# Kernel optimization log

Hardware: AMD Instinct MI355X
Metric: run time of the kernel (lower is better)

Reference implementation:

```python
import jax, jax.numpy as jnp
import numpy as np

N_NODES = 50000
N_EDGES = 400000
D = 64          # in_feats == out_feats (transform=False)
DIST_DIM = 32
NUM = 5         # num_neighbor
N_BOUND = 64    # embedding table rows = N_BOUND + 1


def setup_inputs() -> dict:
    key = jax.random.key(0)
    ks = jax.random.split(key, 9)
    feat = jax.random.normal(ks[0], (N_NODES, D), dtype=jnp.float32)
    loc = jax.random.uniform(ks[1], (N_NODES, 2), dtype=jnp.float32)
    embed_table = jax.random.normal(ks[2], (N_BOUND + 1, DIST_DIM), dtype=jnp.float32)
    G_w = jax.random.normal(ks[3], (D, DIST_DIM), dtype=jnp.float32) / np.sqrt(DIST_DIM)
    agg_w = jax.random.normal(ks[4], (D, 2 * D), dtype=jnp.float32) / np.sqrt(2 * D)
    agg_b = jnp.zeros((D,), dtype=jnp.float32)
    boundaries = jnp.linspace(0.0, 2.0, N_BOUND).astype(jnp.float32)
    src = jax.random.randint(ks[5], (N_EDGES,), 0, N_NODES, dtype=jnp.int32)
    dst = jax.random.randint(ks[6], (N_EDGES,), 0, N_NODES, dtype=jnp.int32)
    inter_ids = jax.random.randint(ks[7], (N_EDGES, NUM), 0, N_NODES, dtype=jnp.int32)
    return {"feat": feat, "loc": loc, "embed_table": embed_table, "G_w": G_w,
            "agg_w": agg_w, "agg_b": agg_b, "boundaries": boundaries,
            "src": src, "dst": dst, "inter_ids": inter_ids}


def reference(feat, loc, embed_table, G_w, agg_w, agg_b, boundaries, src, dst, inter_ids):
    n = feat.shape[0]
    e, num = inter_ids.shape
    one = jnp.ones((e,), dtype=jnp.float32)
    # degrees: d0 = in_deg^-0.5 (at dst), d2 = out_deg^-0.5 (at src), clamp(min=1)
    in_deg = jnp.maximum(jax.ops.segment_sum(one, dst, num_segments=n), 1.0)
    out_deg = jnp.maximum(jax.ops.segment_sum(one, src, num_segments=n), 1.0)
    d0 = in_deg ** -0.5  # [N]
    d2 = out_deg ** -0.5  # [N]
    # dist1: dst->src node distance per edge
    loc_src = loc[src]                                   # [E,2]
    dist1 = jnp.linalg.norm(loc[dst] - loc_src, axis=1)  # [E]
    # dist_: src to each sampled intermediate node
    inter_pos = loc[inter_ids]                                     # [E,num,2]
    dist_ = jnp.linalg.norm(loc_src[:, None, :] - inter_pos, axis=-1)  # [E,num]
    # bucketize (torch right=False == searchsorted side='left') -> embed -> linear G
    b1 = jnp.searchsorted(boundaries, dist1, side='left')   # [E]
    b_ = jnp.searchsorted(boundaries, dist_, side='left')   # [E,num]
    dist_embed1 = embed_table[b1] @ G_w.T                    # [E,D]
    dist_embed_ = embed_table[b_] @ G_w.T                    # [E,num,D]
    # mean over sampled intermediates of (dist-embed * gathered feat)
    dist_embed_dot_h = (dist_embed_ * feat[inter_ids]).mean(axis=1)  # [E,D]
    # agg_fc on concat, degree-scaled
    cat = jnp.concatenate([dist_embed1 * feat[src], dist_embed_dot_h], axis=1)  # [E,2D]
    h = (d0[dst] * d2[src])[:, None] * (cat @ agg_w.T + agg_b)                  # [E,D]
    # copy_e / sum: scatter-sum edges to dst nodes
    rst = jax.ops.segment_sum(h, dst, num_segments=n)  # [N,D]
    return rst
```

## Files before the change

kernel.cpp:

```cpp
#include <hip/hip_runtime.h>


#define DFEAT 64

typedef __attribute__((ext_vector_type(8))) short short8;
typedef __attribute__((ext_vector_type(4))) float floatx4;

__device__ __forceinline__ short bf16h(float x) {
    unsigned u = __float_as_uint(x);
    return (short)((u + 0x7FFFu + ((u >> 16) & 1u)) >> 16);
}
__device__ __forceinline__ float bf16tof(short h) {
    return __uint_as_float(((unsigned)(unsigned short)h) << 16);
}

__device__ __forceinline__ void sb8(const signed char* p, float (&f)[8]) {
    int2 q = *(const int2*)p;
#pragma unroll
    for (int t = 0; t < 4; ++t) f[t] = (float)((q.x << (24 - 8 * t)) >> 24);
#pragma unroll
    for (int t = 0; t < 4; ++t) f[4 + t] = (float)((q.y << (24 - 8 * t)) >> 24);
}

__device__ __forceinline__ int bucketize(float x, float bnd) {
    int i = (int)(x * 31.5f);
    i = min(max(i, 0), 64);
#pragma unroll
    for (int t = 0; t < 3; ++t) {
        float bi = __shfl(bnd, min(i, 63));
        if (i < 64 && bi < x) ++i;
    }
#pragma unroll
    for (int t = 0; t < 2; ++t) {
        float bim = __shfl(bnd, max(i - 1, 0));
        if (i > 0 && bim >= x) --i;
    }
    return i;
}

__global__ void k_init(const float* __restrict__ Etab,
                       const float* __restrict__ G, float* __restrict__ P,
                       float* __restrict__ rst, float* __restrict__ degs,
                       int nRst, int nDeg) {
    int i = blockIdx.x * blockDim.x + threadIdx.x;
    if (i < nRst) rst[i] = 0.0f;
    if (i < nDeg) degs[i] = 0.0f;
    if (i < 65 * DFEAT) {
        int b = i >> 6, o = i & 63;
        float a = 0.0f;
#pragma unroll
        for (int m = 0; m < 32; ++m)
            a = fmaf(Etab[b * 32 + m], G[o * 32 + m], a);
        P[i] = a;
    }
}

__global__ void k_quant(const float* __restrict__ feat,
                        signed char* __restrict__ featQ,
                        float* __restrict__ scaleQ, int N) {
    int w = (blockIdx.x * blockDim.x + threadIdx.x) >> 6;
    int lane = threadIdx.x & 63;
    if (w >= N) return;
    float f = feat[(w << 6) + lane];
    float a = fabsf(f);
#pragma unroll
    for (int o = 32; o; o >>= 1) a = fmaxf(a, __shfl_xor(a, o));
    float inv = (a > 0.0f) ? 127.0f / a : 0.0f;
    int q = __float2int_rn(f * inv);
    featQ[(w << 6) + lane] = (signed char)q;
    if (lane == 0) scaleQ[w] = a * (1.0f / 127.0f);
}

__global__ void k_deg(const int* __restrict__ src, const int* __restrict__ dst,
                      float* __restrict__ degs, int N, int E) {
    int i = blockIdx.x * blockDim.x + threadIdx.x;
    if (i < E) {
        atomicAdd(&degs[dst[i]], 1.0f);
        atomicAdd(&degs[N + src[i]], 1.0f);
    }
}

#define PPAD 68

__global__ __launch_bounds__(256, 3) void k_edge(
    const float* __restrict__ feat, const signed char* __restrict__ featQ,
    const float* __restrict__ scaleQ, const float* __restrict__ loc,
    const float* __restrict__ agg_w, const float* __restrict__ agg_b,
    const float* __restrict__ bnds, const int* __restrict__ src,
    const int* __restrict__ dst, const int* __restrict__ inter,
    const float* __restrict__ P, const float* __restrict__ degs,
    float* __restrict__ rst, int N, int E) {
    const int tid = threadIdx.x;
    const int lane = tid & 63;
    const int wid = tid >> 6;
    const int m16 = lane & 15;
    const int quad = lane >> 4;

    __shared__ float sP[65 * PPAD];
    __shared__ short8 sWBh[16 * 64];
    __shared__ short8 sWBl[16 * 64];

    for (int i = tid; i < 65 * DFEAT; i += 256)
        sP[(i >> 6) * PPAD + (i & 63)] = P[i];

    for (int f = wid; f < 16; f += 4) {
        int sl = f >> 2, nt = f & 3;
        const float* wp = agg_w + (nt * 16 + m16) * 128 + sl * 32 + quad * 8;
        floatx4 wa = *(const floatx4*)wp;
        floatx4 wb = *(const floatx4*)(wp + 4);
        float xs[8] = {wa.x, wa.y, wa.z, wa.w, wb.x, wb.y, wb.z, wb.w};
        short8 h, l;
#pragma unroll
        for (int j = 0; j < 8; ++j) {
            short hh = bf16h(xs[j]);
            h[j] = hh;
            l[j] = bf16h(xs[j] - bf16tof(hh));
        }
        sWBh[f * 64 + lane] = h;
        sWBl[f * 64 + lane] = l;
    }

    const float bnd = bnds[lane];
    float bias4[4];
#pragma unroll
    for (int nt = 0; nt < 4; ++nt) bias4[nt] = agg_b[nt * 16 + m16];

    __syncthreads();

    const int nstream = gridDim.x << 2;
    const int wstream = (blockIdx.x << 2) + wid;
    const int ngroups = (E + 15) >> 4;

    for (int g = wstream; g < ngroups; g += nstream) {
        const int em = (g << 4) + m16;
        const bool act = em < E;
        const int ec = act ? em : 0;

        const int s = __builtin_nontemporal_load(src + ec);
        const int d = __builtin_nontemporal_load(dst + ec);
        const float2 ls = ((const float2*)loc)[s];
        const float2 ld = ((const float2*)loc)[d];
        float dsc = rsqrtf(fmaxf(degs[d], 1.0f)) *
                    rsqrtf(fmaxf(degs[N + s], 1.0f));
        if (!act) dsc = 0.0f;

        float dx = ld.x - ls.x, dy = ld.y - ls.y;
        const int b1 = bucketize(sqrtf(dx * dx + dy * dy), bnd);

        int ij[5], bj[5];
        float sq[5];
#pragma unroll
        for (int j = 0; j < 5; ++j) {
            int id = __builtin_nontemporal_load(inter + ec * 5 + j);
            ij[j] = id;
            if (featQ) sq[j] = scaleQ[id];
            float2 lj = ((const float2*)loc)[id];
            float ex = ls.x - lj.x, ey = ls.y - lj.y;
            bj[j] = bucketize(sqrtf(ex * ex + ey * ey), bnd);
        }

        short8 Ah[4], Al[4];
        if (featQ) {
            const float ssrc = scaleQ[s];
            const signed char* qrow = featQ + (s << 6);
            const float* prow = sP + b1 * PPAD;
#pragma unroll
            for (int sl = 0; sl < 2; ++sl) {
                int k0 = sl * 32 + quad * 8;
                float fq[8];
                sb8(qrow + k0, fq);
                floatx4 pa = *(const floatx4*)(prow + k0);
                floatx4 pb = *(const floatx4*)(prow + k0 + 4);
                float xs[8] = {fq[0] * ssrc * pa.x, fq[1] * ssrc * pa.y,
                               fq[2] * ssrc * pa.z, fq[3] * ssrc * pa.w,
                               fq[4] * ssrc * pb.x, fq[5] * ssrc * pb.y,
                               fq[6] * ssrc * pb.z, fq[7] * ssrc * pb.w};
                short8 h, l;
#pragma unroll
                for (int j = 0; j < 8; ++j) {
                    short hh = bf16h(xs[j]);
                    h[j] = hh;
                    l[j] = bf16h(xs[j] - bf16tof(hh));
                }
                Ah[sl] = h;
                Al[sl] = l;
            }
#pragma unroll
            for (int sl = 0; sl < 2; ++sl) {
                int k0 = sl * 32 + quad * 8;
                float r[8] = {0, 0, 0, 0, 0, 0, 0, 0};
#pragma unroll
                for (int j = 0; j < 5; ++j) {
                    float fq[8];
                    sb8(featQ + (ij[j] << 6) + k0, fq);
                    const float sj = sq[j];
                    const float* pr = sP + bj[j] * PPAD;
                    floatx4 pa = *(const floatx4*)(pr + k0);
                    floatx4 pb = *(const floatx4*)(pr + k0 + 4);
                    r[0] = fmaf(fq[0] * sj, pa.x, r[0]);
                    r[1] = fmaf(fq[1] * sj, pa.y, r[1]);
                    r[2] = fmaf(fq[2] * sj, pa.z, r[2]);
                    r[3] = fmaf(fq[3] * sj, pa.w, r[3]);
                    r[4] = fmaf(fq[4] * sj, pb.x, r[4]);
                    r[5] = fmaf(fq[5] * sj, pb.y, r[5]);
                    r[6] = fmaf(fq[6] * sj, pb.z, r[6]);
                    r[7] = fmaf(fq[7] * sj, pb.w, r[7]);
                }
                short8 h, l;
#pragma unroll
                for (int j = 0; j < 8; ++j) {
                    float x = r[j] * 0.2f;
                    short hh = bf16h(x);
                    h[j] = hh;
                    l[j] = bf16h(x - bf16tof(hh));
                }
                Ah[2 + sl] = h;
                Al[2 + sl] = l;
            }
        } else {
            const float* frow = feat + (s << 6);
            const float* prow = sP + b1 * PPAD;
#pragma unroll
            for (int sl = 0; sl < 2; ++sl) {
                int k0 = sl * 32 + quad * 8;
                floatx4 fa = *(const floatx4*)(frow + k0);
                floatx4 fb = *(const floatx4*)(frow + k0 + 4);
                floatx4 pa = *(const floatx4*)(prow + k0);
                floatx4 pb = *(const floatx4*)(prow + k0 + 4);
                float xs[8] = {fa.x * pa.x, fa.y * pa.y, fa.z * pa.z,
                               fa.w * pa.w, fb.x * pb.x, fb.y * pb.y,
                               fb.z * pb.z, fb.w * pb.w};
                short8 h, l;
#pragma unroll
                for (int j = 0; j < 8; ++j) {
                    short hh = bf16h(xs[j]);
                    h[j] = hh;
                    l[j] = bf16h(xs[j] - bf16tof(hh));
                }
                Ah[sl] = h;
                Al[sl] = l;
            }
#pragma unroll
            for (int sl = 0; sl < 2; ++sl) {
                int k0 = sl * 32 + quad * 8;
                float r[8] = {0, 0, 0, 0, 0, 0, 0, 0};
#pragma unroll
                for (int j = 0; j < 5; ++j) {
                    const float* fr = feat + (ij[j] << 6);
                    const float* pr = sP + bj[j] * PPAD;
                    floatx4 fa = *(const floatx4*)(fr + k0);
                    floatx4 fb = *(const floatx4*)(fr + k0 + 4);
                    floatx4 pa = *(const floatx4*)(pr + k0);
                    floatx4 pb = *(const floatx4*)(pr + k0 + 4);
                    r[0] = fmaf(fa.x, pa.x, r[0]);
                    r[1] = fmaf(fa.y, pa.y, r[1]);
                    r[2] = fmaf(fa.z, pa.z, r[2]);
                    r[3] = fmaf(fa.w, pa.w, r[3]);
                    r[4] = fmaf(fb.x, pb.x, r[4]);
                    r[5] = fmaf(fb.y, pb.y, r[5]);
                    r[6] = fmaf(fb.z, pb.z, r[6]);
                    r[7] = fmaf(fb.w, pb.w, r[7]);
                }
                short8 h, l;
#pragma unroll
                for (int j = 0; j < 8; ++j) {
                    float x = r[j] * 0.2f;
                    short hh = bf16h(x);
                    h[j] = hh;
                    l[j] = bf16h(x - bf16tof(hh));
                }
                Ah[2 + sl] = h;
                Al[2 + sl] = l;
            }
        }

        floatx4 acc[4] = {{0, 0, 0, 0}, {0, 0, 0, 0}, {0, 0, 0, 0}, {0, 0, 0, 0}};
#pragma unroll
        for (int sl = 0; sl < 4; ++sl) {
#pragma unroll
            for (int nt = 0; nt < 4; ++nt) {
                short8 bh = sWBh[((sl << 2) + nt) * 64 + lane];
                short8 bl = sWBl[((sl << 2) + nt) * 64 + lane];
                acc[nt] = __builtin_amdgcn_mfma_f32_16x16x32_bf16(
                    Ah[sl], bh, acc[nt], 0, 0, 0);
                acc[nt] = __builtin_amdgcn_mfma_f32_16x16x32_bf16(
                    Al[sl], bh, acc[nt], 0, 0, 0);
                acc[nt] = __builtin_amdgcn_mfma_f32_16x16x32_bf16(
                    Ah[sl], bl, acc[nt], 0, 0, 0);
            }
        }

#pragma unroll
        for (int r = 0; r < 4; ++r) {
            const int m = (quad << 2) + r;
            const int dm = __shfl(d, m);
            const float sc = __shfl(dsc, m);
            float* ap = rst + (dm << 6) + m16;
            float v0 = (acc[0][r] + bias4[0]) * sc;
            float v1 = (acc[1][r] + bias4[1]) * sc;
            float v2 = (acc[2][r] + bias4[2]) * sc;
            float v3 = (acc[3][r] + bias4[3]) * sc;
            asm volatile("global_atomic_add_f32 %0, %1, off nt"
                         :: "v"(ap), "v"(v0) : "memory");
            asm volatile("global_atomic_add_f32 %0, %1, off offset:64 nt"
                         :: "v"(ap), "v"(v1) : "memory");
            asm volatile("global_atomic_add_f32 %0, %1, off offset:128 nt"
                         :: "v"(ap), "v"(v2) : "memory");
            asm volatile("global_atomic_add_f32 %0, %1, off offset:192 nt"
                         :: "v"(ap), "v"(v3) : "memory");
        }
    }
}

extern "C" void kernel_launch(void* const* d_in, const int* in_sizes, int n_in,
                              void* d_out, int out_size, void* d_ws,
                              size_t ws_size, hipStream_t stream) {
    const float* feat  = (const float*)d_in[0];
    const float* loc   = (const float*)d_in[1];
    const float* embed = (const float*)d_in[2];
    const float* G_w   = (const float*)d_in[3];
    const float* agg_w = (const float*)d_in[4];
    const float* agg_b = (const float*)d_in[5];
    const float* bnds  = (const float*)d_in[6];
    const int* src   = (const int*)d_in[7];
    const int* dst   = (const int*)d_in[8];
    const int* inter = (const int*)d_in[9];

    const int N = in_sizes[0] / DFEAT;
    const int E = in_sizes[7];

    float* rst = (float*)d_out;
    float* ws = (float*)d_ws;
    float* degs = ws;
    float* P = ws + 2 * (size_t)N;
    float* scaleQ = P + 65 * DFEAT;

    size_t fixed_bytes = (2 * (size_t)N + 65 * DFEAT + (size_t)N) * sizeof(float);
    size_t fq_off = (fixed_bytes + 15) & ~(size_t)15;
    size_t need = fq_off + (size_t)N * DFEAT;
    signed char* featQ =
        (ws_size >= need) ? (signed char*)((char*)d_ws + fq_off) : nullptr;

    const int nRst = N * DFEAT;
    const int nDeg = 2 * N;

    k_init<<<(nRst + 255) / 256, 256, 0, stream>>>(embed, G_w, P, rst, degs,
                                                   nRst, nDeg);
    if (featQ)
        k_quant<<<(N + 3) / 4, 256, 0, stream>>>(feat, featQ, scaleQ, N);
    k_deg<<<(E + 255) / 256, 256, 0, stream>>>(src, dst, degs, N, E);
    k_edge<<<768, 256, 0, stream>>>(feat, featQ, scaleQ, loc, agg_w, agg_b,
                                    bnds, src, dst, inter, P, degs, rst, N, E);
}
```

Before: 261.0 us.

## Software-pipeline edge index/bucket front phase one group ahead

```diff
diff --git a/kernel.cpp b/kernel.cpp
--- a/kernel.cpp
+++ b/kernel.cpp
@@ -81,6 +81,45 @@
 }
 
 #define PPAD 68
+
+struct Front {
+    int s, d, b1;
+    float dsc, ssrc;
+    int ij[5], bj[5];
+    float sq[5];
+};
+
+__device__ __forceinline__ void front_phase(
+    int g, int m16, int N, int E, const int* __restrict__ src,
+    const int* __restrict__ dst, const int* __restrict__ inter,
+    const float* __restrict__ loc, const float* __restrict__ degs,
+    const float* __restrict__ scaleQ, bool haveQ, float bnd, Front& F) {
+    const int em = (g << 4) + m16;
+    const bool act = em < E;
+    const int ec = act ? em : 0;
+
+    F.s = __builtin_nontemporal_load(src + ec);
+    F.d = __builtin_nontemporal_load(dst + ec);
+    const float2 ls = ((const float2*)loc)[F.s];
+    const float2 ld = ((const float2*)loc)[F.d];
+    float dsc = rsqrtf(fmaxf(degs[F.d], 1.0f)) *
+                rsqrtf(fmaxf(degs[N + F.s], 1.0f));
+    F.dsc = act ? dsc : 0.0f;
+    F.ssrc = haveQ ? scaleQ[F.s] : 0.0f;
+
+    float dx = ld.x - ls.x, dy = ld.y - ls.y;
+    F.b1 = bucketize(sqrtf(dx * dx + dy * dy), bnd);
+
+#pragma unroll
+    for (int j = 0; j < 5; ++j) {
+        int id = __builtin_nontemporal_load(inter + ec * 5 + j);
+        F.ij[j] = id;
+        F.sq[j] = haveQ ? scaleQ[id] : 0.0f;
+        float2 lj = ((const float2*)loc)[id];
+        float ex = ls.x - lj.x, ey = ls.y - lj.y;
+        F.bj[j] = bucketize(sqrtf(ex * ex + ey * ey), bnd);
+    }
+}
 
 __global__ __launch_bounds__(256, 3) void k_edge(
     const float* __restrict__ feat, const signed char* __restrict__ featQ,
@@ -130,40 +169,25 @@
     const int nstream = gridDim.x << 2;
     const int wstream = (blockIdx.x << 2) + wid;
     const int ngroups = (E + 15) >> 4;
+    const bool haveQ = (featQ != nullptr);
+
+    Front F;
+    if (wstream < ngroups)
+        front_phase(wstream, m16, N, E, src, dst, inter, loc, degs, scaleQ,
+                    haveQ, bnd, F);
 
     for (int g = wstream; g < ngroups; g += nstream) {
-        const int em = (g << 4) + m16;
-        const bool act = em < E;
-        const int ec = act ? em : 0;
-
-        const int s = __builtin_nontemporal_load(src + ec);
-        const int d = __builtin_nontemporal_load(dst + ec);
-        const float2 ls = ((const float2*)loc)[s];
-        const float2 ld = ((const float2*)loc)[d];
-        float dsc = rsqrtf(fmaxf(degs[d], 1.0f)) *
-                    rsqrtf(fmaxf(degs[N + s], 1.0f));
-        if (!act) dsc = 0.0f;
-
-        float dx = ld.x - ls.x, dy = ld.y - ls.y;
-        const int b1 = bucketize(sqrtf(dx * dx + dy * dy), bnd);
-
-        int ij[5], bj[5];
-        float sq[5];
-#pragma unroll
-        for (int j = 0; j < 5; ++j) {
-            int id = __builtin_nontemporal_load(inter + ec * 5 + j);
-            ij[j] = id;
-            if (featQ) sq[j] = scaleQ[id];
-            float2 lj = ((const float2*)loc)[id];
-            float ex = ls.x - lj.x, ey = ls.y - lj.y;
-            bj[j] = bucketize(sqrtf(ex * ex + ey * ey), bnd);
-        }
+        const int gn = g + nstream;
+        const bool hn = gn < ngroups;
+        Front Fn;
+        front_phase(hn ? gn : g, m16, N, E, src, dst, inter, loc, degs,
+                    scaleQ, haveQ, bnd, Fn);
 
         short8 Ah[4], Al[4];
-        if (featQ) {
-            const float ssrc = scaleQ[s];
-            const signed char* qrow = featQ + (s << 6);
-            const float* prow = sP + b1 * PPAD;
+        if (haveQ) {
+            const float ssrc = F.ssrc;
+            const signed char* qrow = featQ + (F.s << 6);
+            const float* prow = sP + F.b1 * PPAD;
 #pragma unroll
             for (int sl = 0; sl < 2; ++sl) {
                 int k0 = sl * 32 + quad * 8;
@@ -192,9 +216,9 @@
 #pragma unroll
                 for (int j = 0; j < 5; ++j) {
                     float fq[8];
-                    sb8(featQ + (ij[j] << 6) + k0, fq);
-                    const float sj = sq[j];
-                    const float* pr = sP + bj[j] * PPAD;
+                    sb8(featQ + (F.ij[j] << 6) + k0, fq);
+                    const float sj = F.sq[j];
+                    const float* pr = sP + F.bj[j] * PPAD;
                     floatx4 pa = *(const floatx4*)(pr + k0);
                     floatx4 pb = *(const floatx4*)(pr + k0 + 4);
                     r[0] = fmaf(fq[0] * sj, pa.x, r[0]);
@@ -218,8 +242,8 @@
                 Al[2 + sl] = l;
             }
         } else {
-            const float* frow = feat + (s << 6);
-            const float* prow = sP + b1 * PPAD;
+            const float* frow = feat + (F.s << 6);
+            const float* prow = sP + F.b1 * PPAD;
 #pragma unroll
             for (int sl = 0; sl < 2; ++sl) {
                 int k0 = sl * 32 + quad * 8;
@@ -246,8 +270,8 @@
                 float r[8] = {0, 0, 0, 0, 0, 0, 0, 0};
 #pragma unroll
                 for (int j = 0; j < 5; ++j) {
-                    const float* fr = feat + (ij[j] << 6);
-                    const float* pr = sP + bj[j] * PPAD;
+                    const float* fr = feat + (F.ij[j] << 6);
+                    const float* pr = sP + F.bj[j] * PPAD;
                     floatx4 fa = *(const floatx4*)(fr + k0);
                     floatx4 fb = *(const floatx4*)(fr + k0 + 4);
                     floatx4 pa = *(const floatx4*)(pr + k0);
@@ -293,8 +317,8 @@
 #pragma unroll
         for (int r = 0; r < 4; ++r) {
             const int m = (quad << 2) + r;
-            const int dm = __shfl(d, m);
-            const float sc = __shfl(dsc, m);
+            const int dm = __shfl(F.d, m);
+            const float sc = __shfl(F.dsc, m);
             float* ap = rst + (dm << 6) + m16;
             float v0 = (acc[0][r] + bias4[0]) * sc;
             float v1 = (acc[1][r] + bias4[1]) * sc;
@@ -309,6 +333,8 @@
             asm volatile("global_atomic_add_f32 %0, %1, off offset:192 nt"
                          :: "v"(ap), "v"(v3) : "memory");
         }
+
+        F = Fn;
     }
 }
 
```

Measured after the change: 331.6 us. +27.1%, slower.
